# Kernel optimization log

Hardware: AMD Instinct MI355X
Metric: run time of the kernel (lower is better)

## Reference

```python
import jax, jax.numpy as jnp
import numpy as np

N_NODES = 50000
N_EDGES = 800000
D = 64          # in_dim == out_dim
K = 3           # kernel_size (number of Gaussian kernels)
PDIM = 1        # pseudo-coordinate dim
EPS = 1e-14


def setup_inputs() -> dict:
    key = jax.random.key(0)
    k = jax.random.split(key, 8)
    x = jax.random.normal(k[0], (N_NODES, D), dtype=jnp.float32)
    edge_index = jax.random.randint(k[1], (2, N_EDGES), 0, N_NODES, dtype=jnp.int64)
    edge_attr = jax.random.uniform(k[2], (N_EDGES, PDIM), dtype=jnp.float32)
    # GMMConv parameters (PyG layout): g [in, K*out], mu [K, dim], sigma [K, dim],
    # root [in, out], bias [out]
    g = jax.random.normal(k[3], (D, K * D), dtype=jnp.float32) / np.sqrt(D)
    mu = jax.random.normal(k[4], (K, PDIM), dtype=jnp.float32)
    sigma = jnp.ones((K, PDIM), dtype=jnp.float32) + 0.1 * jax.random.normal(k[5], (K, PDIM), dtype=jnp.float32)
    root = jax.random.normal(k[6], (D, D), dtype=jnp.float32) / np.sqrt(D)
    bias = jnp.zeros((D,), dtype=jnp.float32)
    return {"x": x, "edge_index": edge_index, "edge_attr": edge_attr,
            "g": g, "mu": mu, "sigma": sigma, "root": root, "bias": bias}


def _gmm_conv(x, src, dst, pseudo, g, mu, sigma, root, bias):
    # per-edge transformed source features: [E, K, D]
    xj = (x[src] @ g).reshape(-1, K, D)
    # Gaussian mixture weights over pseudo-coordinates: [E, K]
    diff = pseudo[:, None, :] - mu[None, :, :]            # [E, K, PDIM]
    gw = jnp.exp((-0.5 * diff * diff / (EPS + sigma * sigma)[None]).sum(-1))
    msg = jnp.einsum('ek,ekd->ed', gw, xj)                # [E, D]
    # mean aggregation at destination nodes
    summed = jax.ops.segment_sum(msg, dst, num_segments=N_NODES)
    cnt = jax.ops.segment_sum(jnp.ones((msg.shape[0],), msg.dtype), dst,
                              num_segments=N_NODES)
    out = summed / jnp.maximum(cnt, 1.0)[:, None]
    return out + x @ root + bias


def reference(x, edge_index, edge_attr, g, mu, sigma, root, bias):
    src, dst = edge_index[0], edge_index[1]
    h = x  # residual shortcut (Identity since in_dim == out_dim)
    out = _gmm_conv(x, src, dst, edge_attr, g, mu, sigma, root, bias)
    # dropout is identity in eval mode
    return jax.nn.silu(out + h)
```

## Files before the change

kernel.cpp:

```cpp
#include <hip/hip_runtime.h>

#define N_NODES 50000
#define N_EDGES 800000
#define NB_SCAN 196

typedef _Float16 f16x8 __attribute__((ext_vector_type(8)));
typedef _Float16 f16x4 __attribute__((ext_vector_type(4)));
typedef float    f32x4 __attribute__((ext_vector_type(4)));

__device__ __forceinline__ unsigned f16bits(float f) {
    const _Float16 h = (_Float16)f;
    return (unsigned)*(const unsigned short*)&h;
}
__device__ __forceinline__ float f16val(unsigned u) {
    const unsigned short us = (unsigned short)u;
    return (float)*(const _Float16*)&us;
}

__global__ void xh_kernel(const float* __restrict__ x, _Float16* __restrict__ xh,
                          int* __restrict__ counts,
                          const float* __restrict__ g, const float* __restrict__ root,
                          _Float16* __restrict__ wfrag) {
    const int i = blockIdx.x * 256 + threadIdx.x;
    if (i < N_NODES) counts[i] = 0;
    if (i < 2048) {
        const int lane = i & 63;
        const int cc   = (i >> 6) & 3;
        const int kc   = i >> 8;
        const int d     = cc * 16 + (lane & 15);
        const int kbase = kc * 32 + (lane >> 4) * 8;
        f16x8 v;
#pragma unroll
        for (int q = 0; q < 8; ++q) {
            const int k = kbase + q;
            const float w = (k < 192) ? g[(k & 63) * 192 + (k >> 6) * 64 + d]
                                      : root[(k - 192) * 64 + d];
            v[q] = (_Float16)w;
        }
        *(f16x8*)&wfrag[(size_t)i * 8] = v;
    }
    if (i >= N_NODES * 16) return;
    const float4 v = *(const float4*)&x[(size_t)i * 4];
    f16x4 h;
    h[0] = (_Float16)v.x; h[1] = (_Float16)v.y;
    h[2] = (_Float16)v.z; h[3] = (_Float16)v.w;
    *(f16x4*)&xh[(size_t)i * 4] = h;
}

__global__ void hist_kernel(const int* __restrict__ ei, int* __restrict__ counts,
                            int* __restrict__ rank) {
    int e = blockIdx.x * 256 + threadIdx.x;
    if (e < N_EDGES) rank[e] = atomicAdd(&counts[ei[N_EDGES + e]], 1);
}

__global__ void scanA_kernel(const int* __restrict__ counts, int* __restrict__ bsum) {
    __shared__ int s[256];
    int i = blockIdx.x * 256 + threadIdx.x;
    s[threadIdx.x] = (i < N_NODES) ? counts[i] : 0;
    __syncthreads();
    for (int d = 128; d > 0; d >>= 1) {
        if (threadIdx.x < d) s[threadIdx.x] += s[threadIdx.x + d];
        __syncthreads();
    }
    if (threadIdx.x == 0) bsum[blockIdx.x] = s[0];
}

__global__ void scanC_kernel(const int* __restrict__ counts, const int* __restrict__ bsum,
                             int* __restrict__ off) {
    __shared__ int s[256];
    __shared__ int rs[256];
    const int tid = threadIdx.x;
    rs[tid] = (tid < NB_SCAN && tid < blockIdx.x) ? bsum[tid] : 0;
    __syncthreads();
    for (int d = 128; d > 0; d >>= 1) {
        if (tid < d) rs[tid] += rs[tid + d];
        __syncthreads();
    }
    const int boff = rs[0];
    const int i = blockIdx.x * 256 + tid;
    const int v = (i < N_NODES) ? counts[i] : 0;
    s[tid] = v;
    __syncthreads();
    for (int d = 1; d < 256; d <<= 1) {
        int t = (tid >= d) ? s[tid - d] : 0;
        __syncthreads();
        s[tid] += t;
        __syncthreads();
    }
    const int excl = s[tid] - v + boff;
    if (i < N_NODES) off[i] = excl;
    if (i == 0) off[N_NODES] = N_EDGES;
}

__global__ void scatter_kernel(const int* __restrict__ ei,
                               const float* __restrict__ pseudo,
                               const int* __restrict__ off,
                               const int* __restrict__ rank,
                               unsigned* __restrict__ packed) {
    int e = blockIdx.x * 256 + threadIdx.x;
    if (e >= N_EDGES) return;
    const int s  = ei[e];
    const int dd = ei[N_EDGES + e];
    const unsigned uq = __float2uint_rn(__saturatef(pseudo[e]) * 65535.0f);
    const int pos = off[dd] + rank[e];
    packed[pos] = (unsigned)s | (uq << 16);
}

__global__ void aggregate_kernel(const _Float16* __restrict__ xh,
                                 const unsigned* __restrict__ packed,
                                 const int* __restrict__ off,
                                 const float* __restrict__ mu,
                                 const float* __restrict__ sigma,
                                 _Float16* __restrict__ aggmh) {
    const int lane = threadIdx.x & 63;
    const int l32  = lane & 31;
    const int half = lane >> 5;
    const int node = blockIdx.x * 4 + (threadIdx.x >> 6);
    if (node >= N_NODES) return;
    const float mu0 = mu[0], mu1 = mu[1], mu2 = mu[2];
    const float s0 = sigma[0], s1 = sigma[1], s2 = sigma[2];
    const float c0 = -0.5f / (1e-14f + s0 * s0);
    const float c1 = -0.5f / (1e-14f + s1 * s1);
    const float c2 = -0.5f / (1e-14f + s2 * s2);
    const int start = off[node], end = off[node + 1];
    float a0lo = 0.f, a0hi = 0.f, a1lo = 0.f, a1hi = 0.f, a2lo = 0.f, a2hi = 0.f;

#define GATH(q)                                                                   \
    const unsigned wae##q = (unsigned)__shfl((int)wa, 2 * (j + q) + half);        \
    const unsigned wbe##q = (unsigned)__shfl((int)wb, 2 * (j + q) + half);        \
    const unsigned xp##q = *(const unsigned*)&xh[(size_t)(wbe##q & 0xFFFFu) * 64 + l32 * 2];
#define ACCU(q)                                                                   \
    {                                                                             \
        const float xlo = f16val(xp##q & 0xFFFFu), xhi = f16val(xp##q >> 16);     \
        const float w0 = f16val(wae##q & 0xFFFFu);                                \
        const float w1 = f16val(wae##q >> 16);                                    \
        const float w2 = f16val(wbe##q >> 16);                                    \
        a0lo += w0 * xlo; a0hi += w0 * xhi;                                       \
        a1lo += w1 * xlo; a1hi += w1 * xhi;                                       \
        a2lo += w2 * xlo; a2hi += w2 * xhi;                                       \
    }

    for (int base = start; base < end; base += 64) {
        const int nrec = min(64, end - base);
        unsigned rec = 0;
        if (lane < nrec) rec = packed[base + lane];
        const float u = (float)(rec >> 16) * (1.0f / 65535.0f);
        const float d0 = u - mu0, d1 = u - mu1, d2 = u - mu2;
        unsigned wa = f16bits(__expf(c0 * d0 * d0))
                    | (f16bits(__expf(c1 * d1 * d1)) << 16);
        unsigned wb = (rec & 0xFFFFu)
                    | (f16bits(__expf(c2 * d2 * d2)) << 16);
        if (lane >= nrec) { wa = 0u; wb = 0u; }
        const int steps = (nrec + 1) >> 1;
        int j = 0;
        for (; j + 4 <= steps; j += 4) {
            GATH(0) GATH(1) GATH(2) GATH(3)
            ACCU(0) ACCU(1) ACCU(2) ACCU(3)
        }
        for (; j < steps; ++j) {
            GATH(0)
            ACCU(0)
        }
    }
#undef GATH
#undef ACCU
    a0lo += __shfl_xor(a0lo, 32); a0hi += __shfl_xor(a0hi, 32);
    a1lo += __shfl_xor(a1lo, 32); a1hi += __shfl_xor(a1hi, 32);
    a2lo += __shfl_xor(a2lo, 32); a2hi += __shfl_xor(a2hi, 32);

    const float inv = 1.0f / fmaxf((float)(end - start), 1.0f);
    _Float16* row = aggmh + (size_t)node * 256;
    if (half == 0) {
        *(unsigned*)&row[2 * l32]      = f16bits(a0lo * inv) | (f16bits(a0hi * inv) << 16);
        *(unsigned*)&row[64 + 2 * l32] = f16bits(a1lo * inv) | (f16bits(a1hi * inv) << 16);
    } else {
        *(unsigned*)&row[128 + 2 * l32] = f16bits(a2lo * inv) | (f16bits(a2hi * inv) << 16);
        *(unsigned*)&row[192 + 2 * l32] = *(const unsigned*)&xh[(size_t)node * 64 + 2 * l32];
    }
}

#define BF(kc, c) (*(const f16x8*)&sWf[((((kc) * 4 + (c)) * 64 + lane) * 8)])
#define MFMA16(a, b, c) __builtin_amdgcn_mfma_f32_16x16x32_f16(a, b, c, 0, 0, 0)
#define COLTILE(c, accv)                                   \
    accv = MFMA16(af0, BF(0, c), accv);                    \
    accv = MFMA16(af1, BF(1, c), accv);                    \
    accv = MFMA16(af2, BF(2, c), accv);                    \
    accv = MFMA16(af3, BF(3, c), accv);                    \
    accv = MFMA16(af4, BF(4, c), accv);                    \
    accv = MFMA16(af5, BF(5, c), accv);                    \
    accv = MFMA16(af6, BF(6, c), accv);                    \
    accv = MFMA16(af7, BF(7, c), accv);
#define EPILOG(c, accv)                                                          \
    {                                                                            \
        const int col = (c) * 16 + (lane & 15);                                  \
        const float bv = bias[col];                                              \
        _Pragma("unroll")                                                        \
        for (int r = 0; r < 4; ++r) {                                            \
            const int rr = orow + r;                                             \
            const float res = (float)aggmh[(size_t)rr * 256 + 192 + col];        \
            const float v = accv[r] + bv + res;                                  \
            out[(size_t)rr * 64 + col] = v / (1.0f + expf(-v));                  \
        }                                                                        \
    }

__global__ __launch_bounds__(256)
void mfma_gemm_kernel(const _Float16* __restrict__ aggmh,
                      const _Float16* __restrict__ wfrag,
                      const float* __restrict__ bias,
                      float* __restrict__ out) {
    __shared__ _Float16 sWf[2048 * 8];
    const int tid = threadIdx.x;
    for (int i = tid; i < 2048; i += 256)
        *(f16x8*)&sWf[i * 8] = *(const f16x8*)&wfrag[(size_t)i * 8];
    __syncthreads();

    const int lane = tid & 63;
    const int wid  = tid >> 6;
    const int row0 = blockIdx.x * 64 + wid * 16;
    if (row0 >= N_NODES) return;

    const size_t abase = (size_t)(row0 + (lane & 15)) * 256 + (lane >> 4) * 8;
    const f16x8 af0 = *(const f16x8*)&aggmh[abase + 0 * 32];
    const f16x8 af1 = *(const f16x8*)&aggmh[abase + 1 * 32];
    const f16x8 af2 = *(const f16x8*)&aggmh[abase + 2 * 32];
    const f16x8 af3 = *(const f16x8*)&aggmh[abase + 3 * 32];
    const f16x8 af4 = *(const f16x8*)&aggmh[abase + 4 * 32];
    const f16x8 af5 = *(const f16x8*)&aggmh[abase + 5 * 32];
    const f16x8 af6 = *(const f16x8*)&aggmh[abase + 6 * 32];
    const f16x8 af7 = *(const f16x8*)&aggmh[abase + 7 * 32];

    f32x4 acc0 = {0.f, 0.f, 0.f, 0.f};
    f32x4 acc1 = {0.f, 0.f, 0.f, 0.f};
    f32x4 acc2 = {0.f, 0.f, 0.f, 0.f};
    f32x4 acc3 = {0.f, 0.f, 0.f, 0.f};
    COLTILE(0, acc0)
    COLTILE(1, acc1)
    COLTILE(2, acc2)
    COLTILE(3, acc3)

    const int orow = row0 + (lane >> 4) * 4;
    EPILOG(0, acc0)
    EPILOG(1, acc1)
    EPILOG(2, acc2)
    EPILOG(3, acc3)
}

extern "C" void kernel_launch(void* const* d_in, const int* in_sizes, int n_in,
                              void* d_out, int out_size, void* d_ws, size_t ws_size,
                              hipStream_t stream) {
    const float* x     = (const float*)d_in[0];
    const int*   ei    = (const int*)d_in[1];
    const float* ea    = (const float*)d_in[2];
    const float* g     = (const float*)d_in[3];
    const float* mu    = (const float*)d_in[4];
    const float* sigma = (const float*)d_in[5];
    const float* root  = (const float*)d_in[6];
    const float* bias  = (const float*)d_in[7];
    float* out = (float*)d_out;

    char* ws = (char*)d_ws;
    const size_t aggmh_bytes  = (size_t)N_NODES * 256 * sizeof(_Float16);
    const size_t xh_bytes     = (size_t)N_NODES * 64 * sizeof(_Float16);
    const size_t packed_bytes = (size_t)N_EDGES * sizeof(unsigned);
    const size_t rank_bytes   = (size_t)N_EDGES * sizeof(int);
    const size_t wfrag_bytes  = (size_t)2048 * 8 * sizeof(_Float16);
    _Float16* aggmh  = (_Float16*)ws;
    _Float16* xh     = (_Float16*)(ws + aggmh_bytes);
    unsigned* packed = (unsigned*)(ws + aggmh_bytes + xh_bytes);
    int*      rank   = (int*)(ws + aggmh_bytes + xh_bytes + packed_bytes);
    _Float16* wfrag  = (_Float16*)(ws + aggmh_bytes + xh_bytes + packed_bytes + rank_bytes);
    int* counts = (int*)(ws + aggmh_bytes + xh_bytes + packed_bytes + rank_bytes + wfrag_bytes);
    int* off    = counts + N_NODES;
    int* bsum   = off + N_NODES + 1;

    xh_kernel<<<(N_NODES * 16 + 255) / 256, 256, 0, stream>>>(x, xh, counts, g, root, wfrag);
    hist_kernel<<<(N_EDGES + 255) / 256, 256, 0, stream>>>(ei, counts, rank);
    scanA_kernel<<<NB_SCAN, 256, 0, stream>>>(counts, bsum);
    scanC_kernel<<<NB_SCAN, 256, 0, stream>>>(counts, bsum, off);
    scatter_kernel<<<(N_EDGES + 255) / 256, 256, 0, stream>>>(ei, ea, off, rank, packed);
    aggregate_kernel<<<(N_NODES + 3) / 4, 256, 0, stream>>>(xh, packed, off, mu, sigma, aggmh);
    mfma_gemm_kernel<<<(N_NODES + 63) / 64, 256, 0, stream>>>(aggmh, wfrag, bias, out);
}
```

Before: 103.9 us.

## Fuse neighbor aggregation and MFMA GEMM into one kernel via shared memory

Merges the aggregation kernel and the MFMA GEMM kernel into a single kernel. Each block aggregates 16 nodes (4 per wave) into a shared-memory tile, then each wave computes one 16-column output tile with MFMA. This removes the round trip of the 25.6 MB fp16 aggmh intermediate through global memory and one kernel launch. In exchange each block holds only 16 rows, so each wave reloads its B fragments from global memory per block, and a block barrier makes all waves wait for the slowest node's aggregation.

```diff
diff --git a/kernel.cpp b/kernel.cpp
--- a/kernel.cpp
+++ b/kernel.cpp
@@ -106,24 +106,27 @@
     packed[pos] = (unsigned)s | (uq << 16);
 }
 
-__global__ void aggregate_kernel(const _Float16* __restrict__ xh,
-                                 const unsigned* __restrict__ packed,
-                                 const int* __restrict__ off,
-                                 const float* __restrict__ mu,
-                                 const float* __restrict__ sigma,
-                                 _Float16* __restrict__ aggmh) {
-    const int lane = threadIdx.x & 63;
+#define MFMA16(a, b, c) __builtin_amdgcn_mfma_f32_16x16x32_f16(a, b, c, 0, 0, 0)
+__global__ __launch_bounds__(256)
+void agg_gemm_kernel(const _Float16* __restrict__ xh,
+                     const unsigned* __restrict__ packed,
+                     const int* __restrict__ off,
+                     const float* __restrict__ mu,
+                     const float* __restrict__ sigma,
+                     const _Float16* __restrict__ wfrag,
+                     const float* __restrict__ bias,
+                     float* __restrict__ out) {
+    __shared__ _Float16 sA[16][264];
+    const int tid  = threadIdx.x;
+    const int lane = tid & 63;
     const int l32  = lane & 31;
     const int half = lane >> 5;
-    const int node = blockIdx.x * 4 + (threadIdx.x >> 6);
-    if (node >= N_NODES) return;
+    const int wid  = tid >> 6;
     const float mu0 = mu[0], mu1 = mu[1], mu2 = mu[2];
     const float s0 = sigma[0], s1 = sigma[1], s2 = sigma[2];
     const float c0 = -0.5f / (1e-14f + s0 * s0);
     const float c1 = -0.5f / (1e-14f + s1 * s1);
     const float c2 = -0.5f / (1e-14f + s2 * s2);
-    const int start = off[node], end = off[node + 1];
-    float a0lo = 0.f, a0hi = 0.f, a1lo = 0.f, a1hi = 0.f, a2lo = 0.f, a2hi = 0.f;
 
 #define GATH(q)                                                                   \
     const unsigned wae##q = (unsigned)__shfl((int)wa, 2 * (j + q) + half);        \
@@ -140,109 +143,89 @@
         a2lo += w2 * xlo; a2hi += w2 * xhi;                                       \
     }
 
-    for (int base = start; base < end; base += 64) {
-        const int nrec = min(64, end - base);
-        unsigned rec = 0;
-        if (lane < nrec) rec = packed[base + lane];
-        const float u = (float)(rec >> 16) * (1.0f / 65535.0f);
-        const float d0 = u - mu0, d1 = u - mu1, d2 = u - mu2;
-        unsigned wa = f16bits(__expf(c0 * d0 * d0))
-                    | (f16bits(__expf(c1 * d1 * d1)) << 16);
-        unsigned wb = (rec & 0xFFFFu)
-                    | (f16bits(__expf(c2 * d2 * d2)) << 16);
-        if (lane >= nrec) { wa = 0u; wb = 0u; }
-        const int steps = (nrec + 1) >> 1;
-        int j = 0;
-        for (; j + 4 <= steps; j += 4) {
-            GATH(0) GATH(1) GATH(2) GATH(3)
-            ACCU(0) ACCU(1) ACCU(2) ACCU(3)
+#pragma unroll 1
+    for (int i = 0; i < 4; ++i) {
+        const int lrow = wid * 4 + i;
+        const int node = blockIdx.x * 16 + lrow;
+        const int start = off[node], end = off[node + 1];
+        float a0lo = 0.f, a0hi = 0.f, a1lo = 0.f, a1hi = 0.f, a2lo = 0.f, a2hi = 0.f;
+        for (int base = start; base < end; base += 64) {
+            const int nrec = min(64, end - base);
+            unsigned rec = 0;
+            if (lane < nrec) rec = packed[base + lane];
+            const float u = (float)(rec >> 16) * (1.0f / 65535.0f);
+            const float d0 = u - mu0, d1 = u - mu1, d2 = u - mu2;
+            unsigned wa = f16bits(__expf(c0 * d0 * d0))
+                        | (f16bits(__expf(c1 * d1 * d1)) << 16);
+            unsigned wb = (rec & 0xFFFFu)
+                        | (f16bits(__expf(c2 * d2 * d2)) << 16);
+            if (lane >= nrec) { wa = 0u; wb = 0u; }
+            const int steps = (nrec + 1) >> 1;
+            int j = 0;
+            for (; j + 4 <= steps; j += 4) {
+                GATH(0) GATH(1) GATH(2) GATH(3)
+                ACCU(0) ACCU(1) ACCU(2) ACCU(3)
+            }
+            for (; j < steps; ++j) {
+                GATH(0)
+                ACCU(0)
+            }
         }
-        for (; j < steps; ++j) {
-            GATH(0)
-            ACCU(0)
+        a0lo += __shfl_xor(a0lo, 32); a0hi += __shfl_xor(a0hi, 32);
+        a1lo += __shfl_xor(a1lo, 32); a1hi += __shfl_xor(a1hi, 32);
+        a2lo += __shfl_xor(a2lo, 32); a2hi += __shfl_xor(a2hi, 32);
+        const float inv = 1.0f / fmaxf((float)(end - start), 1.0f);
+        if (half == 0) {
+            *(unsigned*)&sA[lrow][2 * l32]      = f16bits(a0lo * inv) | (f16bits(a0hi * inv) << 16);
+            *(unsigned*)&sA[lrow][64 + 2 * l32] = f16bits(a1lo * inv) | (f16bits(a1hi * inv) << 16);
+        } else {
+            *(unsigned*)&sA[lrow][128 + 2 * l32] = f16bits(a2lo * inv) | (f16bits(a2hi * inv) << 16);
+            *(unsigned*)&sA[lrow][192 + 2 * l32] = *(const unsigned*)&xh[(size_t)node * 64 + 2 * l32];
         }
     }
 #undef GATH
 #undef ACCU
-    a0lo += __shfl_xor(a0lo, 32); a0hi += __shfl_xor(a0hi, 32);
-    a1lo += __shfl_xor(a1lo, 32); a1hi += __shfl_xor(a1hi, 32);
-    a2lo += __shfl_xor(a2lo, 32); a2hi += __shfl_xor(a2hi, 32);
-
-    const float inv = 1.0f / fmaxf((float)(end - start), 1.0f);
-    _Float16* row = aggmh + (size_t)node * 256;
-    if (half == 0) {
-        *(unsigned*)&row[2 * l32]      = f16bits(a0lo * inv) | (f16bits(a0hi * inv) << 16);
-        *(unsigned*)&row[64 + 2 * l32] = f16bits(a1lo * inv) | (f16bits(a1hi * inv) << 16);
-    } else {
-        *(unsigned*)&row[128 + 2 * l32] = f16bits(a2lo * inv) | (f16bits(a2hi * inv) << 16);
-        *(unsigned*)&row[192 + 2 * l32] = *(const unsigned*)&xh[(size_t)node * 64 + 2 * l32];
-    }
-}
-
-#define BF(kc, c) (*(const f16x8*)&sWf[((((kc) * 4 + (c)) * 64 + lane) * 8)])
-#define MFMA16(a, b, c) __builtin_amdgcn_mfma_f32_16x16x32_f16(a, b, c, 0, 0, 0)
-#define COLTILE(c, accv)                                   \
-    accv = MFMA16(af0, BF(0, c), accv);                    \
-    accv = MFMA16(af1, BF(1, c), accv);                    \
-    accv = MFMA16(af2, BF(2, c), accv);                    \
-    accv = MFMA16(af3, BF(3, c), accv);                    \
-    accv = MFMA16(af4, BF(4, c), accv);                    \
-    accv = MFMA16(af5, BF(5, c), accv);                    \
-    accv = MFMA16(af6, BF(6, c), accv);                    \
-    accv = MFMA16(af7, BF(7, c), accv);
-#define EPILOG(c, accv)                                                          \
-    {                                                                            \
-        const int col = (c) * 16 + (lane & 15);                                  \
-        const float bv = bias[col];                                              \
-        _Pragma("unroll")                                                        \
-        for (int r = 0; r < 4; ++r) {                                            \
-            const int rr = orow + r;                                             \
-            const float res = (float)aggmh[(size_t)rr * 256 + 192 + col];        \
-            const float v = accv[r] + bv + res;                                  \
-            out[(size_t)rr * 64 + col] = v / (1.0f + expf(-v));                  \
-        }                                                                        \
-    }
-
-__global__ __launch_bounds__(256)
-void mfma_gemm_kernel(const _Float16* __restrict__ aggmh,
-                      const _Float16* __restrict__ wfrag,
-                      const float* __restrict__ bias,
-                      float* __restrict__ out) {
-    __shared__ _Float16 sWf[2048 * 8];
-    const int tid = threadIdx.x;
-    for (int i = tid; i < 2048; i += 256)
-        *(f16x8*)&sWf[i * 8] = *(const f16x8*)&wfrag[(size_t)i * 8];
-    __syncthreads();
-
-    const int lane = tid & 63;
-    const int wid  = tid >> 6;
-    const int row0 = blockIdx.x * 64 + wid * 16;
-    if (row0 >= N_NODES) return;
-
-    const size_t abase = (size_t)(row0 + (lane & 15)) * 256 + (lane >> 4) * 8;
-    const f16x8 af0 = *(const f16x8*)&aggmh[abase + 0 * 32];
-    const f16x8 af1 = *(const f16x8*)&aggmh[abase + 1 * 32];
-    const f16x8 af2 = *(const f16x8*)&aggmh[abase + 2 * 32];
-    const f16x8 af3 = *(const f16x8*)&aggmh[abase + 3 * 32];
-    const f16x8 af4 = *(const f16x8*)&aggmh[abase + 4 * 32];
-    const f16x8 af5 = *(const f16x8*)&aggmh[abase + 5 * 32];
-    const f16x8 af6 = *(const f16x8*)&aggmh[abase + 6 * 32];
-    const f16x8 af7 = *(const f16x8*)&aggmh[abase + 7 * 32];
-
-    f32x4 acc0 = {0.f, 0.f, 0.f, 0.f};
-    f32x4 acc1 = {0.f, 0.f, 0.f, 0.f};
-    f32x4 acc2 = {0.f, 0.f, 0.f, 0.f};
-    f32x4 acc3 = {0.f, 0.f, 0.f, 0.f};
-    COLTILE(0, acc0)
-    COLTILE(1, acc1)
-    COLTILE(2, acc2)
-    COLTILE(3, acc3)
-
-    const int orow = row0 + (lane >> 4) * 4;
-    EPILOG(0, acc0)
-    EPILOG(1, acc1)
-    EPILOG(2, acc2)
-    EPILOG(3, acc3)
+    __syncthreads();
+
+    const int r  = lane & 15;
+    const int kq = lane >> 4;
+    const f16x8 af0 = *(const f16x8*)&sA[r][0 * 32 + kq * 8];
+    const f16x8 af1 = *(const f16x8*)&sA[r][1 * 32 + kq * 8];
+    const f16x8 af2 = *(const f16x8*)&sA[r][2 * 32 + kq * 8];
+    const f16x8 af3 = *(const f16x8*)&sA[r][3 * 32 + kq * 8];
+    const f16x8 af4 = *(const f16x8*)&sA[r][4 * 32 + kq * 8];
+    const f16x8 af5 = *(const f16x8*)&sA[r][5 * 32 + kq * 8];
+    const f16x8 af6 = *(const f16x8*)&sA[r][6 * 32 + kq * 8];
+    const f16x8 af7 = *(const f16x8*)&sA[r][7 * 32 + kq * 8];
+    const f16x8 bf0 = *(const f16x8*)&wfrag[(size_t)((0 * 4 + wid) * 64 + lane) * 8];
+    const f16x8 bf1 = *(const f16x8*)&wfrag[(size_t)((1 * 4 + wid) * 64 + lane) * 8];
+    const f16x8 bf2 = *(const f16x8*)&wfrag[(size_t)((2 * 4 + wid) * 64 + lane) * 8];
+    const f16x8 bf3 = *(const f16x8*)&wfrag[(size_t)((3 * 4 + wid) * 64 + lane) * 8];
+    const f16x8 bf4 = *(const f16x8*)&wfrag[(size_t)((4 * 4 + wid) * 64 + lane) * 8];
+    const f16x8 bf5 = *(const f16x8*)&wfrag[(size_t)((5 * 4 + wid) * 64 + lane) * 8];
+    const f16x8 bf6 = *(const f16x8*)&wfrag[(size_t)((6 * 4 + wid) * 64 + lane) * 8];
+    const f16x8 bf7 = *(const f16x8*)&wfrag[(size_t)((7 * 4 + wid) * 64 + lane) * 8];
+
+    f32x4 acc = {0.f, 0.f, 0.f, 0.f};
+    acc = MFMA16(af0, bf0, acc);
+    acc = MFMA16(af1, bf1, acc);
+    acc = MFMA16(af2, bf2, acc);
+    acc = MFMA16(af3, bf3, acc);
+    acc = MFMA16(af4, bf4, acc);
+    acc = MFMA16(af5, bf5, acc);
+    acc = MFMA16(af6, bf6, acc);
+    acc = MFMA16(af7, bf7, acc);
+
+    const int col = wid * 16 + r;
+    const float bv = bias[col];
+    const int lrow0 = (lane >> 4) * 4;
+#pragma unroll
+    for (int q = 0; q < 4; ++q) {
+        const int lr = lrow0 + q;
+        const float res = (float)sA[lr][192 + col];
+        const float v = acc[q] + bv + res;
+        out[(size_t)(blockIdx.x * 16 + lr) * 64 + col] = v / (1.0f + expf(-v));
+    }
 }
 
 extern "C" void kernel_launch(void* const* d_in, const int* in_sizes, int n_in,
@@ -259,17 +242,15 @@
     float* out = (float*)d_out;
 
     char* ws = (char*)d_ws;
-    const size_t aggmh_bytes  = (size_t)N_NODES * 256 * sizeof(_Float16);
     const size_t xh_bytes     = (size_t)N_NODES * 64 * sizeof(_Float16);
     const size_t packed_bytes = (size_t)N_EDGES * sizeof(unsigned);
     const size_t rank_bytes   = (size_t)N_EDGES * sizeof(int);
     const size_t wfrag_bytes  = (size_t)2048 * 8 * sizeof(_Float16);
-    _Float16* aggmh  = (_Float16*)ws;
-    _Float16* xh     = (_Float16*)(ws + aggmh_bytes);
-    unsigned* packed = (unsigned*)(ws + aggmh_bytes + xh_bytes);
-    int*      rank   = (int*)(ws + aggmh_bytes + xh_bytes + packed_bytes);
-    _Float16* wfrag  = (_Float16*)(ws + aggmh_bytes + xh_bytes + packed_bytes + rank_bytes);
-    int* counts = (int*)(ws + aggmh_bytes + xh_bytes + packed_bytes + rank_bytes + wfrag_bytes);
+    _Float16* xh     = (_Float16*)ws;
+    unsigned* packed = (unsigned*)(ws + xh_bytes);
+    int*      rank   = (int*)(ws + xh_bytes + packed_bytes);
+    _Float16* wfrag  = (_Float16*)(ws + xh_bytes + packed_bytes + rank_bytes);
+    int* counts = (int*)(ws + xh_bytes + packed_bytes + rank_bytes + wfrag_bytes);
     int* off    = counts + N_NODES;
     int* bsum   = off + N_NODES + 1;
 
@@ -278,6 +259,5 @@
     scanA_kernel<<<NB_SCAN, 256, 0, stream>>>(counts, bsum);
     scanC_kernel<<<NB_SCAN, 256, 0, stream>>>(counts, bsum, off);
     scatter_kernel<<<(N_EDGES + 255) / 256, 256, 0, stream>>>(ei, ea, off, rank, packed);
-    aggregate_kernel<<<(N_NODES + 3) / 4, 256, 0, stream>>>(xh, packed, off, mu, sigma, aggmh);
-    mfma_gemm_kernel<<<(N_NODES + 63) / 64, 256, 0, stream>>>(aggmh, wfrag, bias, out);
-}
+    agg_gemm_kernel<<<N_NODES / 16, 256, 0, stream>>>(xh, packed, off, mu, sigma, wfrag, bias, out);
+}
```

Measured after the change: 99.77 us, median of 2. -3.9%, faster.
